# Optimization experiments

Measured on AMD Instinct MI355X. Metric: run time of the kernel, lower is better.

## Reference

```python
import jax, jax.numpy as jnp
import numpy as np

B, L, H, NH = 4, 1024, 768, 12
NE, M, P = 30, 6, 600
EMB, BS, NC = 768, 16, 97
NEG = -1e30


def setup_inputs() -> dict:
    key = jax.random.key(0)
    ks = jax.random.split(key, 9)
    sequence_output = jax.random.normal(ks[0], (B, L, H), jnp.float32)
    attention = jax.random.uniform(ks[1], (B, NH, L, L), jnp.float32)
    mention_idx = jax.random.randint(ks[2], (B, NE, M), 0, L)
    mention_mask = jnp.ones((B, NE, M), jnp.float32)
    hts = jax.random.randint(ks[3], (B, P, 2), 0, NE)
    s = 0.02
    head_W = jax.random.normal(ks[4], (EMB, 2 * H), jnp.float32) * s
    head_b = jnp.zeros((EMB,), jnp.float32)
    tail_W = jax.random.normal(ks[5], (EMB, 2 * H), jnp.float32) * s
    tail_b = jnp.zeros((EMB,), jnp.float32)
    proj_W = jax.random.normal(ks[6], (H, EMB * BS), jnp.float32) * s
    cls_W = jax.random.normal(ks[7], (NC, H), jnp.float32) * s
    cls_b = jnp.zeros((NC,), jnp.float32)
    return {
        'sequence_output': sequence_output, 'attention': attention,
        'head_W': head_W, 'head_b': head_b, 'tail_W': tail_W, 'tail_b': tail_b,
        'proj_W': proj_W, 'cls_W': cls_W, 'cls_b': cls_b,
        'mention_mask': mention_mask, 'mention_idx': mention_idx, 'hts': hts,
    }


def reference(sequence_output, attention, head_W, head_b, tail_W, tail_b,
              proj_W, cls_W, cls_b, mention_mask, mention_idx, hts):
    b_, l_, h_ = sequence_output.shape
    bidx = jnp.arange(b_)[:, None, None]                     # [B,1,1]
    # ---- per-entity pooling (segment reduce over ragged mentions) ----
    m_emb = sequence_output[bidx, mention_idx]               # [B,NE,M,H]
    att_t = attention.transpose(0, 2, 1, 3)                  # [B,L,NH,L]
    m_att = att_t[bidx, mention_idx]                         # [B,NE,M,NH,L]
    masked = jnp.where(mention_mask[..., None] > 0, m_emb, NEG)
    e_emb = jax.nn.logsumexp(masked, axis=2)                 # [B,NE,H]
    cnt = jnp.maximum(mention_mask.sum(2), 1.0)              # [B,NE]
    e_att = (m_att * mention_mask[..., None, None]).sum(2) / cnt[..., None, None]  # [B,NE,NH,L]
    # ---- head/tail gathers over pairs ----
    b2 = jnp.arange(b_)[:, None]                             # [B,1]
    h_emb = e_emb[b2, hts[..., 0]]                           # [B,P,H]
    t_emb = e_emb[b2, hts[..., 1]]
    h_att = e_att[b2, hts[..., 0]]                           # [B,P,NH,L]
    t_att = e_att[b2, hts[..., 1]]
    ht_att = (h_att * t_att).mean(2)                         # [B,P,L]
    ht_att = ht_att / (ht_att.sum(-1, keepdims=True) + 1e-30)
    rs = jnp.einsum('bpl,blh->bph', ht_att, sequence_output) # [B,P,H]
    # ---- extractors + block-bilinear classifier ----
    hs = jnp.tanh(jnp.concatenate([h_emb, rs], -1) @ head_W.T + head_b)  # [B,P,EMB]
    ts = jnp.tanh(jnp.concatenate([t_emb, rs], -1) @ tail_W.T + tail_b)
    emb = hs.shape[-1]
    bs = proj_W.shape[1] // emb
    p_ = hs.shape[1]
    b1 = hs.reshape(b_, p_, emb // bs, bs)
    b2t = ts.reshape(b_, p_, emb // bs, bs)
    bl = (b1[..., :, None] * b2t[..., None, :]).reshape(b_, p_, emb * bs)
    logits = (bl @ proj_W.T) @ cls_W.T + cls_b               # [B,P,NC]
    return logits
```

## Files before the change

kernel.cpp:

```cpp
#include <hip/hip_runtime.h>
#include <cmath>

#define B_   4
#define L_   1024
#define H_   768
#define NH_  12
#define NE_  30
#define M_   6
#define P_   600
#define EMB_ 768
#define BS_  16
#define NC_  97

typedef __bf16 bf16x8 __attribute__((ext_vector_type(8)));
typedef float floatx4 __attribute__((ext_vector_type(4)));

union V16 { uint4 q; __bf16 b[8]; bf16x8 v; };
union V8  { unsigned long long u; __bf16 b[4]; };


__global__ __launch_bounds__(256) void k_entity_pool(
    const float* __restrict__ seq, const float* __restrict__ mmask,
    const int* __restrict__ midx, __bf16* __restrict__ e_embB)
{
  int be = blockIdx.x;
  int tid = threadIdx.x;
  int idx[M_]; float msk[M_];
#pragma unroll
  for (int m = 0; m < M_; ++m) {
    idx[m] = midx[be * M_ + m];
    msk[m] = mmask[be * M_ + m];
  }
  int b = be / NE_;
  const float* sb = seq + (size_t)b * L_ * H_;
  for (int h = tid; h < H_; h += 256) {
    float v[M_]; float mx = -3.0e38f;
#pragma unroll
    for (int m = 0; m < M_; ++m) {
      float x = (msk[m] > 0.f) ? sb[(size_t)idx[m] * H_ + h] : -1e30f;
      v[m] = x; mx = fmaxf(mx, x);
    }
    float s = 0.f;
#pragma unroll
    for (int m = 0; m < M_; ++m) s += expf(v[m] - mx);
    e_embB[(size_t)be * H_ + h] = (__bf16)(mx + logf(s));
  }
}

__global__ __launch_bounds__(256) void k_entity_att(
    const float* __restrict__ att, const float* __restrict__ mmask,
    const int* __restrict__ midx, __bf16* __restrict__ e_att)
{
  int i = blockIdx.x * 256 + threadIdx.x;
  int l4 = (i & 255) * 4;
  int nh = (i >> 8) % NH_;
  int be = i / (256 * NH_);
  int b  = be / NE_;
  float s0=0.f, s1=0.f, s2=0.f, s3=0.f, cnt=0.f;
#pragma unroll
  for (int m = 0; m < M_; ++m) {
    float mk = mmask[be*M_ + m];
    cnt += mk;
    int id = midx[be*M_ + m];
    float4 a = *reinterpret_cast<const float4*>(
        att + (((size_t)b*NH_ + nh)*L_ + id)*L_ + l4);
    s0 += mk*a.x; s1 += mk*a.y; s2 += mk*a.z; s3 += mk*a.w;
  }
  float inv = 1.f / fmaxf(cnt, 1.f);
  V8 o;
  o.b[0]=(__bf16)(s0*inv); o.b[1]=(__bf16)(s1*inv);
  o.b[2]=(__bf16)(s2*inv); o.b[3]=(__bf16)(s3*inv);
  *reinterpret_cast<unsigned long long*>(e_att + ((size_t)be*NH_ + nh)*L_ + l4) = o.u;
}

__global__ __launch_bounds__(256) void k_htatt(
    const __bf16* __restrict__ e_att, const int* __restrict__ hts,
    __bf16* __restrict__ htatt)
{
  int bp = blockIdx.x;
  int b = bp / P_;
  int tid = threadIdx.x;
  int hi = hts[bp*2 + 0], ti = hts[bp*2 + 1];
  const __bf16* ha = e_att + (size_t)(b*NE_ + hi) * NH_ * L_;
  const __bf16* ta = e_att + (size_t)(b*NE_ + ti) * NH_ * L_;
  int l4 = tid * 4;
  float v[4] = {0.f,0.f,0.f,0.f};
#pragma unroll
  for (int nh = 0; nh < NH_; ++nh) {
    V8 x, y;
    x.u = *reinterpret_cast<const unsigned long long*>(ha + nh*L_ + l4);
    y.u = *reinterpret_cast<const unsigned long long*>(ta + nh*L_ + l4);
#pragma unroll
    for (int q = 0; q < 4; ++q) v[q] += (float)x.b[q] * (float)y.b[q];
  }
  float loc = 0.f;
#pragma unroll
  for (int q = 0; q < 4; ++q) { v[q] *= (1.f/NH_); loc += v[q]; }
  __shared__ float red[4];
  for (int off = 32; off > 0; off >>= 1) loc += __shfl_down(loc, off, 64);
  if ((tid & 63) == 0) red[tid >> 6] = loc;
  __syncthreads();
  float inv = 1.f / (red[0] + red[1] + red[2] + red[3] + 1e-30f);
  V8 o;
#pragma unroll
  for (int q = 0; q < 4; ++q) o.b[q] = (__bf16)(v[q] * inv);
  *reinterpret_cast<unsigned long long*>(htatt + (size_t)bp*L_ + l4) = o.u;
}

__global__ __launch_bounds__(256) void k_cvt_weights(
    const float* __restrict__ headW, const float* __restrict__ tailW,
    const float* __restrict__ clsW, __bf16* __restrict__ Wt,
    __bf16* __restrict__ clsA)
{
  int gid = blockIdx.x*256 + threadIdx.x;
  if (gid < 2*H_*384) {
    int sel = gid / (H_*384);
    int rem = gid % (H_*384);
    int o = rem / 384;
    int k4 = (rem % 384) * 4;
    const float* W = sel ? tailW : headW;
    float4 v = *reinterpret_cast<const float4*>(W + (long)o*(2*H_) + k4);
    V8 d; d.b[0]=(__bf16)v.x; d.b[1]=(__bf16)v.y; d.b[2]=(__bf16)v.z; d.b[3]=(__bf16)v.w;
    *reinterpret_cast<unsigned long long*>(Wt + ((long)sel*H_ + o)*(2*H_) + k4) = d.u;
  } else {
    int rem = gid - 2*H_*384;
    int row = rem / 192;
    int k4 = (rem % 192) * 4;
    V8 d;
    if (row < NC_) {
      float4 v = *reinterpret_cast<const float4*>(clsW + (long)row*H_ + k4);
      d.b[0]=(__bf16)v.x; d.b[1]=(__bf16)v.y; d.b[2]=(__bf16)v.z; d.b[3]=(__bf16)v.w;
    } else {
      d.b[0]=d.b[1]=d.b[2]=d.b[3]=(__bf16)0.f;
    }
    *reinterpret_cast<unsigned long long*>(clsA + (long)row*H_ + k4) = d.u;
  }
}

__global__ __launch_bounds__(256) void k_transpose_bf(
    const float* __restrict__ in, __bf16* __restrict__ out,
    int R, int C, long inStride, long outStride)
{
  __shared__ float t[32][33];
  long ib = (long)blockIdx.z * inStride, ob = (long)blockIdx.z * outStride;
  int c0 = blockIdx.x*32, r0 = blockIdx.y*32;
  int tx = threadIdx.x & 31, ty = threadIdx.x >> 5;
#pragma unroll
  for (int p = 0; p < 4; ++p)
    t[ty + p*8][tx] = in[ib + (long)(r0 + ty + p*8)*C + c0 + tx];
  __syncthreads();
#pragma unroll
  for (int p = 0; p < 4; ++p)
    out[ob + (long)(c0 + ty + p*8)*R + r0 + tx] = (__bf16)t[tx][ty + p*8];
}

__device__ __forceinline__ void gemm_core(
    const __bf16* __restrict__ A, int lda, long aRow0,
    const __bf16* __restrict__ Bt, int ldb, long bRow0,
    int K, __bf16* sm, floatx4 acc[2][2])
{
  const int tid = threadIdx.x;
  const int lid = tid & 63, w = tid >> 6;
  const int ar = (w & 1) * 32, bc = (w >> 1) * 32;
  const int frow = lid & 15, kg = lid >> 4;
  __bf16* As = sm;
  __bf16* Bs = sm + 64*40;
  const int srow = tid >> 2, skq = (tid & 3) * 8;
  const __bf16* ag = A + (aRow0 + srow) * (long)lda + skq;
  const __bf16* bg = Bt + (bRow0 + srow) * (long)ldb + skq;
  for (int k0 = 0; k0 < K; k0 += 32) {
    uint4 av = *reinterpret_cast<const uint4*>(ag + k0);
    uint4 bv = *reinterpret_cast<const uint4*>(bg + k0);
    __syncthreads();
    *reinterpret_cast<uint4*>(As + srow*40 + skq) = av;
    *reinterpret_cast<uint4*>(Bs + srow*40 + skq) = bv;
    __syncthreads();
    V16 a0, a1, b0, b1;
    a0.q = *reinterpret_cast<const uint4*>(As + (ar + frow)*40 + kg*8);
    a1.q = *reinterpret_cast<const uint4*>(As + (ar + 16 + frow)*40 + kg*8);
    b0.q = *reinterpret_cast<const uint4*>(Bs + (bc + frow)*40 + kg*8);
    b1.q = *reinterpret_cast<const uint4*>(Bs + (bc + 16 + frow)*40 + kg*8);
    acc[0][0] = __builtin_amdgcn_mfma_f32_16x16x32_bf16(a0.v, b0.v, acc[0][0], 0, 0, 0);
    acc[0][1] = __builtin_amdgcn_mfma_f32_16x16x32_bf16(a0.v, b1.v, acc[0][1], 0, 0, 0);
    acc[1][0] = __builtin_amdgcn_mfma_f32_16x16x32_bf16(a1.v, b0.v, acc[1][0], 0, 0, 0);
    acc[1][1] = __builtin_amdgcn_mfma_f32_16x16x32_bf16(a1.v, b1.v, acc[1][1], 0, 0, 0);
  }
}

__global__ __launch_bounds__(256) void k_rs_mfma(
    const __bf16* __restrict__ htatt, const __bf16* __restrict__ seqT,
    __bf16* __restrict__ rs)
{
  __shared__ __bf16 sm[2*64*40];
  int b = blockIdx.z, p0 = blockIdx.y*64, h0 = blockIdx.x*64;
  floatx4 acc[2][2] = {};
  gemm_core(htatt, L_, (long)b*P_ + p0, seqT + (long)b*H_*L_, L_, h0, L_, sm, acc);
  int lid = threadIdx.x & 63, w = threadIdx.x >> 6;
  int ar = (w&1)*32, bc = (w>>1)*32, frow = lid&15, kg = lid>>4;
#pragma unroll
  for (int i = 0; i < 2; ++i)
#pragma unroll
    for (int r = 0; r < 4; ++r) {
      int p = p0 + ar + i*16 + kg*4 + r;
      if (p < P_) {
#pragma unroll
        for (int j = 0; j < 2; ++j)
          rs[((long)b*P_ + p)*H_ + h0 + bc + j*16 + frow] = (__bf16)acc[i][j][r];
      }
    }
}

__global__ __launch_bounds__(256) void k_pre_mfma(
    const __bf16* __restrict__ e_embB, const __bf16* __restrict__ Wt,
    float* __restrict__ hpre, float* __restrict__ tpre)
{
  __shared__ __bf16 sm[2*64*40];
  int sel = blockIdx.z, r0 = blockIdx.y*64, o0 = blockIdx.x*64;
  floatx4 acc[2][2] = {};
  gemm_core(e_embB, H_, r0, Wt + (long)sel*H_*(2*H_), 2*H_, o0, H_, sm, acc);
  float* out = sel ? tpre : hpre;
  int lid = threadIdx.x & 63, w = threadIdx.x >> 6;
  int ar = (w&1)*32, bc = (w>>1)*32, frow = lid&15, kg = lid>>4;
#pragma unroll
  for (int i = 0; i < 2; ++i)
#pragma unroll
    for (int r = 0; r < 4; ++r) {
      int be = r0 + ar + i*16 + kg*4 + r;
      if (be < B_*NE_) {
#pragma unroll
        for (int j = 0; j < 2; ++j)
          out[(long)be*EMB_ + o0 + bc + j*16 + frow] = acc[i][j][r];
      }
    }
}

__global__ __launch_bounds__(256) void k_extract_mfma(
    const __bf16* __restrict__ rs, const __bf16* __restrict__ Wt,
    const float* __restrict__ headb, const float* __restrict__ tailb,
    const float* __restrict__ hpre, const float* __restrict__ tpre,
    const int* __restrict__ hts, __bf16* __restrict__ hs, __bf16* __restrict__ ts)
{
  __shared__ __bf16 sm[2*64*40];
  int sel = blockIdx.z, r0 = blockIdx.y*64, o0 = blockIdx.x*64;
  const float* bias = sel ? tailb : headb;
  const float* pre = sel ? tpre : hpre;
  __bf16* out = sel ? ts : hs;
  floatx4 acc[2][2] = {};
  gemm_core(rs, H_, r0, Wt + (long)sel*H_*(2*H_) + H_, 2*H_, o0, H_, sm, acc);
  int lid = threadIdx.x & 63, w = threadIdx.x >> 6;
  int ar = (w&1)*32, bc = (w>>1)*32, frow = lid&15, kg = lid>>4;
#pragma unroll
  for (int i = 0; i < 2; ++i)
#pragma unroll
    for (int r = 0; r < 4; ++r) {
      int row = r0 + ar + i*16 + kg*4 + r;
      if (row < B_*P_) {
        int b = row / P_;
        int e = hts[row*2 + sel];
        const float* prow = pre + (long)(b*NE_ + e) * EMB_;
#pragma unroll
        for (int j = 0; j < 2; ++j) {
          int o = o0 + bc + j*16 + frow;
          out[(long)row*EMB_ + o] = (__bf16)tanhf(acc[i][j][r] + prow[o] + bias[o]);
        }
      }
    }
}

__global__ __launch_bounds__(256) void k_wc_mfma(
    const __bf16* __restrict__ clsA, const __bf16* __restrict__ projWT,
    __bf16* __restrict__ WcT)
{
  __shared__ __bf16 sm[2*64*40];
  int n0 = blockIdx.x*64, r0 = blockIdx.y*64;
  floatx4 acc[2][2] = {};
  gemm_core(clsA, H_, r0, projWT, H_, n0, H_, sm, acc);
  int lid = threadIdx.x & 63, w = threadIdx.x >> 6;
  int ar = (w&1)*32, bc = (w>>1)*32, frow = lid&15, kg = lid>>4;
#pragma unroll
  for (int i = 0; i < 2; ++i)
#pragma unroll
    for (int r = 0; r < 4; ++r) {
      int c = r0 + ar + i*16 + kg*4 + r;
#pragma unroll
      for (int j = 0; j < 2; ++j)
        WcT[(long)c*(EMB_*BS_) + n0 + bc + j*16 + frow] = (__bf16)acc[i][j][r];
    }
}

__global__ __launch_bounds__(512) void k_logits_mfma(
    const __bf16* __restrict__ hs, const __bf16* __restrict__ ts,
    const __bf16* __restrict__ WcT, float* __restrict__ partial)
{
  int r0 = blockIdx.x * 16;
  int kh = blockIdx.y;
  int tid = threadIdx.x;
  int w = tid >> 6, lid = tid & 63;
  int frow = lid & 15, kg = lid >> 4;
  int row = r0 + frow;
  long hsrow = (long)row * EMB_;
  floatx4 acc[7] = {};
  int kbase0 = kh*3072 + w*384;
  for (int s = 0; s < 12; ++s) {
    int kb = kbase0 + s*32 + kg*8;
    int q16 = (kb >> 8) << 4;
    int ii = (kb >> 4) & 15;
    int jj0 = kb & 15;
    float hv = (float)hs[hsrow + q16 + ii];
    V16 tsv; tsv.q = *reinterpret_cast<const uint4*>(ts + hsrow + q16 + jj0);
    bf16x8 af;
#pragma unroll
    for (int j = 0; j < 8; ++j) af[j] = (__bf16)(hv * (float)tsv.b[j]);
#pragma unroll
    for (int f = 0; f < 7; ++f) {
      V16 bv; bv.q = *reinterpret_cast<const uint4*>(WcT + (long)(f*16 + frow)*(EMB_*BS_) + kb);
      acc[f] = __builtin_amdgcn_mfma_f32_16x16x32_bf16(af, bv.v, acc[f], 0, 0, 0);
    }
  }
  __shared__ float red[8][16][112];
#pragma unroll
  for (int f = 0; f < 7; ++f)
#pragma unroll
    for (int r = 0; r < 4; ++r)
      red[w][kg*4 + r][f*16 + frow] = acc[f][r];
  __syncthreads();
  for (int e = tid; e < 16*112; e += 512) {
    int rr = e / 112, cc = e % 112;
    float s = 0.f;
#pragma unroll
    for (int ww = 0; ww < 8; ++ww) s += red[ww][rr][cc];
    partial[((long)kh*B_*P_ + r0 + rr)*112 + cc] = s;
  }
}

__global__ __launch_bounds__(256) void k_lred(
    const float* __restrict__ partial, const float* __restrict__ clsb,
    float* __restrict__ out)
{
  int gid = blockIdx.x*256 + threadIdx.x;
  if (gid >= B_*P_*112) return;
  int row = gid / 112, c = gid % 112;
  if (c < NC_) {
    float s = clsb[c];
#pragma unroll
    for (int q = 0; q < 4; ++q)
      s += partial[((long)q*B_*P_ + row)*112 + c];
    out[(long)row*NC_ + c] = s;
  }
}

extern "C" void kernel_launch(void* const* d_in, const int* in_sizes, int n_in,
                              void* d_out, int out_size, void* d_ws, size_t ws_size,
                              hipStream_t stream) {
  const float* seq   = (const float*)d_in[0];
  const float* att   = (const float*)d_in[1];
  const float* headW = (const float*)d_in[2];
  const float* headb = (const float*)d_in[3];
  const float* tailW = (const float*)d_in[4];
  const float* tailb = (const float*)d_in[5];
  const float* projW = (const float*)d_in[6];
  const float* clsW  = (const float*)d_in[7];
  const float* clsb  = (const float*)d_in[8];
  const float* mmask = (const float*)d_in[9];
  const int* midx = (const int*)d_in[10];
  const int* hts  = (const int*)d_in[11];

  char* p = (char*)d_ws;
  auto alloc_f = [&](size_t n){ float* r = (float*)p; p += n*sizeof(float); return r; };
  auto alloc_b = [&](size_t n){ __bf16* r = (__bf16*)p; p += n*2; return r; };
  float* hpre    = alloc_f((size_t)B_*NE_*EMB_);
  float* tpre    = alloc_f((size_t)B_*NE_*EMB_);
  float* partial = alloc_f((size_t)4*B_*P_*112);
  __bf16* e_embB = alloc_b((size_t)128*H_);
  __bf16* e_att  = alloc_b((size_t)B_*NE_*NH_*L_);
  __bf16* htattb = alloc_b((size_t)2464*L_);
  __bf16* seqT   = alloc_b((size_t)B_*H_*L_);
  __bf16* rsb    = alloc_b((size_t)2432*H_);
  __bf16* Wt     = alloc_b((size_t)2*H_*2*H_);
  __bf16* clsA   = alloc_b((size_t)128*H_);
  __bf16* WcT    = alloc_b((size_t)128*EMB_*BS_);
  __bf16* projWT = alloc_b((size_t)EMB_*BS_*H_);
  __bf16* hsb = projWT;
  __bf16* tsb = projWT + (size_t)B_*P_*EMB_;

  k_cvt_weights<<<2400, 256, 0, stream>>>(headW, tailW, clsW, Wt, clsA);
  k_transpose_bf<<<dim3(EMB_*BS_/32, H_/32, 1), 256, 0, stream>>>(
      projW, projWT, H_, EMB_*BS_, 0, 0);
  k_wc_mfma<<<dim3(EMB_*BS_/64, 2), 256, 0, stream>>>(clsA, projWT, WcT);
  k_entity_pool<<<B_*NE_, 256, 0, stream>>>(seq, mmask, midx, e_embB);
  k_entity_att<<<(B_*NE_*NH_*256)/256, 256, 0, stream>>>(att, mmask, midx, e_att);
  k_transpose_bf<<<dim3(H_/32, L_/32, B_), 256, 0, stream>>>(
      seq, seqT, L_, H_, (long)L_*H_, (long)H_*L_);
  k_htatt<<<B_*P_, 256, 0, stream>>>(e_att, hts, htattb);
  k_rs_mfma<<<dim3(H_/64, 10, B_), 256, 0, stream>>>(htattb, seqT, rsb);
  k_pre_mfma<<<dim3(EMB_/64, 2, 2), 256, 0, stream>>>(e_embB, Wt, hpre, tpre);
  k_extract_mfma<<<dim3(EMB_/64, 38, 2), 256, 0, stream>>>(
      rsb, Wt, headb, tailb, hpre, tpre, hts, hsb, tsb);
  k_logits_mfma<<<dim3(150, 4), 512, 0, stream>>>(hsb, tsb, WcT, partial);
  k_lred<<<(B_*P_*112 + 255)/256, 256, 0, stream>>>(partial, clsb, (float*)d_out);
}
```

Measured before the change: 455.2 us.

## Merge independent prep and mid stages into combined kernels; drop logits split-K reduction

```diff
diff --git a/kernel.cpp b/kernel.cpp
--- a/kernel.cpp
+++ b/kernel.cpp
@@ -17,142 +17,6 @@
 
 union V16 { uint4 q; __bf16 b[8]; bf16x8 v; };
 union V8  { unsigned long long u; __bf16 b[4]; };
-
-
-__global__ __launch_bounds__(256) void k_entity_pool(
-    const float* __restrict__ seq, const float* __restrict__ mmask,
-    const int* __restrict__ midx, __bf16* __restrict__ e_embB)
-{
-  int be = blockIdx.x;
-  int tid = threadIdx.x;
-  int idx[M_]; float msk[M_];
-#pragma unroll
-  for (int m = 0; m < M_; ++m) {
-    idx[m] = midx[be * M_ + m];
-    msk[m] = mmask[be * M_ + m];
-  }
-  int b = be / NE_;
-  const float* sb = seq + (size_t)b * L_ * H_;
-  for (int h = tid; h < H_; h += 256) {
-    float v[M_]; float mx = -3.0e38f;
-#pragma unroll
-    for (int m = 0; m < M_; ++m) {
-      float x = (msk[m] > 0.f) ? sb[(size_t)idx[m] * H_ + h] : -1e30f;
-      v[m] = x; mx = fmaxf(mx, x);
-    }
-    float s = 0.f;
-#pragma unroll
-    for (int m = 0; m < M_; ++m) s += expf(v[m] - mx);
-    e_embB[(size_t)be * H_ + h] = (__bf16)(mx + logf(s));
-  }
-}
-
-__global__ __launch_bounds__(256) void k_entity_att(
-    const float* __restrict__ att, const float* __restrict__ mmask,
-    const int* __restrict__ midx, __bf16* __restrict__ e_att)
-{
-  int i = blockIdx.x * 256 + threadIdx.x;
-  int l4 = (i & 255) * 4;
-  int nh = (i >> 8) % NH_;
-  int be = i / (256 * NH_);
-  int b  = be / NE_;
-  float s0=0.f, s1=0.f, s2=0.f, s3=0.f, cnt=0.f;
-#pragma unroll
-  for (int m = 0; m < M_; ++m) {
-    float mk = mmask[be*M_ + m];
-    cnt += mk;
-    int id = midx[be*M_ + m];
-    float4 a = *reinterpret_cast<const float4*>(
-        att + (((size_t)b*NH_ + nh)*L_ + id)*L_ + l4);
-    s0 += mk*a.x; s1 += mk*a.y; s2 += mk*a.z; s3 += mk*a.w;
-  }
-  float inv = 1.f / fmaxf(cnt, 1.f);
-  V8 o;
-  o.b[0]=(__bf16)(s0*inv); o.b[1]=(__bf16)(s1*inv);
-  o.b[2]=(__bf16)(s2*inv); o.b[3]=(__bf16)(s3*inv);
-  *reinterpret_cast<unsigned long long*>(e_att + ((size_t)be*NH_ + nh)*L_ + l4) = o.u;
-}
-
-__global__ __launch_bounds__(256) void k_htatt(
-    const __bf16* __restrict__ e_att, const int* __restrict__ hts,
-    __bf16* __restrict__ htatt)
-{
-  int bp = blockIdx.x;
-  int b = bp / P_;
-  int tid = threadIdx.x;
-  int hi = hts[bp*2 + 0], ti = hts[bp*2 + 1];
-  const __bf16* ha = e_att + (size_t)(b*NE_ + hi) * NH_ * L_;
-  const __bf16* ta = e_att + (size_t)(b*NE_ + ti) * NH_ * L_;
-  int l4 = tid * 4;
-  float v[4] = {0.f,0.f,0.f,0.f};
-#pragma unroll
-  for (int nh = 0; nh < NH_; ++nh) {
-    V8 x, y;
-    x.u = *reinterpret_cast<const unsigned long long*>(ha + nh*L_ + l4);
-    y.u = *reinterpret_cast<const unsigned long long*>(ta + nh*L_ + l4);
-#pragma unroll
-    for (int q = 0; q < 4; ++q) v[q] += (float)x.b[q] * (float)y.b[q];
-  }
-  float loc = 0.f;
-#pragma unroll
-  for (int q = 0; q < 4; ++q) { v[q] *= (1.f/NH_); loc += v[q]; }
-  __shared__ float red[4];
-  for (int off = 32; off > 0; off >>= 1) loc += __shfl_down(loc, off, 64);
-  if ((tid & 63) == 0) red[tid >> 6] = loc;
-  __syncthreads();
-  float inv = 1.f / (red[0] + red[1] + red[2] + red[3] + 1e-30f);
-  V8 o;
-#pragma unroll
-  for (int q = 0; q < 4; ++q) o.b[q] = (__bf16)(v[q] * inv);
-  *reinterpret_cast<unsigned long long*>(htatt + (size_t)bp*L_ + l4) = o.u;
-}
-
-__global__ __launch_bounds__(256) void k_cvt_weights(
-    const float* __restrict__ headW, const float* __restrict__ tailW,
-    const float* __restrict__ clsW, __bf16* __restrict__ Wt,
-    __bf16* __restrict__ clsA)
-{
-  int gid = blockIdx.x*256 + threadIdx.x;
-  if (gid < 2*H_*384) {
-    int sel = gid / (H_*384);
-    int rem = gid % (H_*384);
-    int o = rem / 384;
-    int k4 = (rem % 384) * 4;
-    const float* W = sel ? tailW : headW;
-    float4 v = *reinterpret_cast<const float4*>(W + (long)o*(2*H_) + k4);
-    V8 d; d.b[0]=(__bf16)v.x; d.b[1]=(__bf16)v.y; d.b[2]=(__bf16)v.z; d.b[3]=(__bf16)v.w;
-    *reinterpret_cast<unsigned long long*>(Wt + ((long)sel*H_ + o)*(2*H_) + k4) = d.u;
-  } else {
-    int rem = gid - 2*H_*384;
-    int row = rem / 192;
-    int k4 = (rem % 192) * 4;
-    V8 d;
-    if (row < NC_) {
-      float4 v = *reinterpret_cast<const float4*>(clsW + (long)row*H_ + k4);
-      d.b[0]=(__bf16)v.x; d.b[1]=(__bf16)v.y; d.b[2]=(__bf16)v.z; d.b[3]=(__bf16)v.w;
-    } else {
-      d.b[0]=d.b[1]=d.b[2]=d.b[3]=(__bf16)0.f;
-    }
-    *reinterpret_cast<unsigned long long*>(clsA + (long)row*H_ + k4) = d.u;
-  }
-}
-
-__global__ __launch_bounds__(256) void k_transpose_bf(
-    const float* __restrict__ in, __bf16* __restrict__ out,
-    int R, int C, long inStride, long outStride)
-{
-  __shared__ float t[32][33];
-  long ib = (long)blockIdx.z * inStride, ob = (long)blockIdx.z * outStride;
-  int c0 = blockIdx.x*32, r0 = blockIdx.y*32;
-  int tx = threadIdx.x & 31, ty = threadIdx.x >> 5;
-#pragma unroll
-  for (int p = 0; p < 4; ++p)
-    t[ty + p*8][tx] = in[ib + (long)(r0 + ty + p*8)*C + c0 + tx];
-  __syncthreads();
-#pragma unroll
-  for (int p = 0; p < 4; ++p)
-    out[ob + (long)(c0 + ty + p*8)*R + r0 + tx] = (__bf16)t[tx][ty + p*8];
-}
 
 __device__ __forceinline__ void gemm_core(
     const __bf16* __restrict__ A, int lda, long aRow0,
@@ -187,6 +51,197 @@
   }
 }
 
+#define S1_CVT  2400
+#define S1_TPW  9216
+#define S1_TPS  3072
+#define S1_POOL 120
+#define S1_ATT  1440
+
+__device__ __forceinline__ void transpose_body(
+    const float* __restrict__ in, __bf16* __restrict__ out,
+    int R, int C, int bx, int by, float (*t)[33])
+{
+  int c0 = bx*32, r0 = by*32;
+  int tx = threadIdx.x & 31, ty = threadIdx.x >> 5;
+#pragma unroll
+  for (int p = 0; p < 4; ++p)
+    t[ty + p*8][tx] = in[(long)(r0 + ty + p*8)*C + c0 + tx];
+  __syncthreads();
+#pragma unroll
+  for (int p = 0; p < 4; ++p)
+    out[(long)(c0 + ty + p*8)*R + r0 + tx] = (__bf16)t[tx][ty + p*8];
+}
+
+__global__ __launch_bounds__(256) void k_prep(
+    const float* __restrict__ seq, const float* __restrict__ att,
+    const float* __restrict__ headW, const float* __restrict__ tailW,
+    const float* __restrict__ projW, const float* __restrict__ clsW,
+    const float* __restrict__ mmask, const int* __restrict__ midx,
+    __bf16* __restrict__ Wt, __bf16* __restrict__ clsA,
+    __bf16* __restrict__ projWT, __bf16* __restrict__ seqT,
+    __bf16* __restrict__ e_embB, __bf16* __restrict__ e_att)
+{
+  __shared__ float t[32][33];
+  int blk = blockIdx.x;
+  int tid = threadIdx.x;
+  if (blk < S1_CVT) {
+    int gid = blk*256 + tid;
+    if (gid < 2*H_*384) {
+      int sel = gid / (H_*384);
+      int rem = gid % (H_*384);
+      int o = rem / 384;
+      int k4 = (rem % 384) * 4;
+      const float* W = sel ? tailW : headW;
+      float4 v = *reinterpret_cast<const float4*>(W + (long)o*(2*H_) + k4);
+      V8 d; d.b[0]=(__bf16)v.x; d.b[1]=(__bf16)v.y; d.b[2]=(__bf16)v.z; d.b[3]=(__bf16)v.w;
+      *reinterpret_cast<unsigned long long*>(Wt + ((long)sel*H_ + o)*(2*H_) + k4) = d.u;
+    } else {
+      int rem = gid - 2*H_*384;
+      int row = rem / 192;
+      int k4 = (rem % 192) * 4;
+      V8 d;
+      if (row < NC_) {
+        float4 v = *reinterpret_cast<const float4*>(clsW + (long)row*H_ + k4);
+        d.b[0]=(__bf16)v.x; d.b[1]=(__bf16)v.y; d.b[2]=(__bf16)v.z; d.b[3]=(__bf16)v.w;
+      } else {
+        d.b[0]=d.b[1]=d.b[2]=d.b[3]=(__bf16)0.f;
+      }
+      *reinterpret_cast<unsigned long long*>(clsA + (long)row*H_ + k4) = d.u;
+    }
+  } else if (blk < S1_CVT + S1_TPW) {
+    int b = blk - S1_CVT;
+    transpose_body(projW, projWT, H_, EMB_*BS_, b % 384, b / 384, t);
+  } else if (blk < S1_CVT + S1_TPW + S1_TPS) {
+    int b = blk - (S1_CVT + S1_TPW);
+    int bx = b % 24, by = (b / 24) % 32, bz = b / (24*32);
+    transpose_body(seq + (long)bz*L_*H_, seqT + (long)bz*H_*L_, L_, H_, bx, by, t);
+  } else if (blk < S1_CVT + S1_TPW + S1_TPS + S1_POOL) {
+    int be = blk - (S1_CVT + S1_TPW + S1_TPS);
+    int idx[M_]; float msk[M_];
+#pragma unroll
+    for (int m = 0; m < M_; ++m) {
+      idx[m] = midx[be * M_ + m];
+      msk[m] = mmask[be * M_ + m];
+    }
+    int b = be / NE_;
+    const float* sb = seq + (size_t)b * L_ * H_;
+    for (int h = tid; h < H_; h += 256) {
+      float v[M_]; float mx = -3.0e38f;
+#pragma unroll
+      for (int m = 0; m < M_; ++m) {
+        float x = (msk[m] > 0.f) ? sb[(size_t)idx[m] * H_ + h] : -1e30f;
+        v[m] = x; mx = fmaxf(mx, x);
+      }
+      float s = 0.f;
+#pragma unroll
+      for (int m = 0; m < M_; ++m) s += expf(v[m] - mx);
+      e_embB[(size_t)be * H_ + h] = (__bf16)(mx + logf(s));
+    }
+  } else {
+    int i = (blk - (S1_CVT + S1_TPW + S1_TPS + S1_POOL))*256 + tid;
+    int l4 = (i & 255) * 4;
+    int nh = (i >> 8) % NH_;
+    int be = i / (256 * NH_);
+    int b  = be / NE_;
+    float s0=0.f, s1=0.f, s2=0.f, s3=0.f, cnt=0.f;
+#pragma unroll
+    for (int m = 0; m < M_; ++m) {
+      float mk = mmask[be*M_ + m];
+      cnt += mk;
+      int id = midx[be*M_ + m];
+      float4 a = *reinterpret_cast<const float4*>(
+          att + (((size_t)b*NH_ + nh)*L_ + id)*L_ + l4);
+      s0 += mk*a.x; s1 += mk*a.y; s2 += mk*a.z; s3 += mk*a.w;
+    }
+    float inv = 1.f / fmaxf(cnt, 1.f);
+    V8 o;
+    o.b[0]=(__bf16)(s0*inv); o.b[1]=(__bf16)(s1*inv);
+    o.b[2]=(__bf16)(s2*inv); o.b[3]=(__bf16)(s3*inv);
+    *reinterpret_cast<unsigned long long*>(e_att + ((size_t)be*NH_ + nh)*L_ + l4) = o.u;
+  }
+}
+
+#define S2_WC  384
+#define S2_HT  2400
+#define S2_PRE 48
+
+__global__ __launch_bounds__(256) void k_mid(
+    const __bf16* __restrict__ clsA, const __bf16* __restrict__ projWT,
+    const __bf16* __restrict__ e_att, const int* __restrict__ hts,
+    const __bf16* __restrict__ e_embB, const __bf16* __restrict__ Wt,
+    __bf16* __restrict__ WcT, __bf16* __restrict__ htatt,
+    float* __restrict__ hpre, float* __restrict__ tpre)
+{
+  __shared__ __bf16 sm[2*64*40];
+  int blk = blockIdx.x;
+  int tid = threadIdx.x;
+  if (blk < S2_WC) {
+    int n0 = (blk % 192)*64, r0 = (blk / 192)*64;
+    floatx4 acc[2][2] = {};
+    gemm_core(clsA, H_, r0, projWT, H_, n0, H_, sm, acc);
+    int lid = tid & 63, w = tid >> 6;
+    int ar = (w&1)*32, bc = (w>>1)*32, frow = lid&15, kg = lid>>4;
+#pragma unroll
+    for (int i = 0; i < 2; ++i)
+#pragma unroll
+      for (int r = 0; r < 4; ++r) {
+        int c = r0 + ar + i*16 + kg*4 + r;
+#pragma unroll
+        for (int j = 0; j < 2; ++j)
+          WcT[(long)c*(EMB_*BS_) + n0 + bc + j*16 + frow] = (__bf16)acc[i][j][r];
+      }
+  } else if (blk < S2_WC + S2_HT) {
+    int bp = blk - S2_WC;
+    int b = bp / P_;
+    int hi = hts[bp*2 + 0], ti = hts[bp*2 + 1];
+    const __bf16* ha = e_att + (size_t)(b*NE_ + hi) * NH_ * L_;
+    const __bf16* ta = e_att + (size_t)(b*NE_ + ti) * NH_ * L_;
+    int l4 = tid * 4;
+    float v[4] = {0.f,0.f,0.f,0.f};
+#pragma unroll
+    for (int nh = 0; nh < NH_; ++nh) {
+      V8 x, y;
+      x.u = *reinterpret_cast<const unsigned long long*>(ha + nh*L_ + l4);
+      y.u = *reinterpret_cast<const unsigned long long*>(ta + nh*L_ + l4);
+#pragma unroll
+      for (int q = 0; q < 4; ++q) v[q] += (float)x.b[q] * (float)y.b[q];
+    }
+    float loc = 0.f;
+#pragma unroll
+    for (int q = 0; q < 4; ++q) { v[q] *= (1.f/NH_); loc += v[q]; }
+    float* red = reinterpret_cast<float*>(sm);
+    for (int off = 32; off > 0; off >>= 1) loc += __shfl_down(loc, off, 64);
+    if ((tid & 63) == 0) red[tid >> 6] = loc;
+    __syncthreads();
+    float inv = 1.f / (red[0] + red[1] + red[2] + red[3] + 1e-30f);
+    V8 o;
+#pragma unroll
+    for (int q = 0; q < 4; ++q) o.b[q] = (__bf16)(v[q] * inv);
+    *reinterpret_cast<unsigned long long*>(htatt + (size_t)bp*L_ + l4) = o.u;
+  } else {
+    int tb = blk - (S2_WC + S2_HT);
+    int o0 = (tb % 12)*64;
+    int r0 = ((tb / 12) & 1)*64;
+    int sel = tb / 24;
+    floatx4 acc[2][2] = {};
+    gemm_core(e_embB, H_, r0, Wt + (long)sel*H_*(2*H_), 2*H_, o0, H_, sm, acc);
+    float* out = sel ? tpre : hpre;
+    int lid = tid & 63, w = tid >> 6;
+    int ar = (w&1)*32, bc = (w>>1)*32, frow = lid&15, kg = lid>>4;
+#pragma unroll
+    for (int i = 0; i < 2; ++i)
+#pragma unroll
+      for (int r = 0; r < 4; ++r) {
+        int be = r0 + ar + i*16 + kg*4 + r;
+        if (be < B_*NE_) {
+#pragma unroll
+          for (int j = 0; j < 2; ++j)
+            out[(long)be*EMB_ + o0 + bc + j*16 + frow] = acc[i][j][r];
+        }
+      }
+  }
+}
+
 __global__ __launch_bounds__(256) void k_rs_mfma(
     const __bf16* __restrict__ htatt, const __bf16* __restrict__ seqT,
     __bf16* __restrict__ rs)
@@ -206,30 +261,6 @@
 #pragma unroll
         for (int j = 0; j < 2; ++j)
           rs[((long)b*P_ + p)*H_ + h0 + bc + j*16 + frow] = (__bf16)acc[i][j][r];
-      }
-    }
-}
-
-__global__ __launch_bounds__(256) void k_pre_mfma(
-    const __bf16* __restrict__ e_embB, const __bf16* __restrict__ Wt,
-    float* __restrict__ hpre, float* __restrict__ tpre)
-{
-  __shared__ __bf16 sm[2*64*40];
-  int sel = blockIdx.z, r0 = blockIdx.y*64, o0 = blockIdx.x*64;
-  floatx4 acc[2][2] = {};
-  gemm_core(e_embB, H_, r0, Wt + (long)sel*H_*(2*H_), 2*H_, o0, H_, sm, acc);
-  float* out = sel ? tpre : hpre;
-  int lid = threadIdx.x & 63, w = threadIdx.x >> 6;
-  int ar = (w&1)*32, bc = (w>>1)*32, frow = lid&15, kg = lid>>4;
-#pragma unroll
-  for (int i = 0; i < 2; ++i)
-#pragma unroll
-    for (int r = 0; r < 4; ++r) {
-      int be = r0 + ar + i*16 + kg*4 + r;
-      if (be < B_*NE_) {
-#pragma unroll
-        for (int j = 0; j < 2; ++j)
-          out[(long)be*EMB_ + o0 + bc + j*16 + frow] = acc[i][j][r];
       }
     }
 }
@@ -267,41 +298,20 @@
     }
 }
 
-__global__ __launch_bounds__(256) void k_wc_mfma(
-    const __bf16* __restrict__ clsA, const __bf16* __restrict__ projWT,
-    __bf16* __restrict__ WcT)
-{
-  __shared__ __bf16 sm[2*64*40];
-  int n0 = blockIdx.x*64, r0 = blockIdx.y*64;
-  floatx4 acc[2][2] = {};
-  gemm_core(clsA, H_, r0, projWT, H_, n0, H_, sm, acc);
-  int lid = threadIdx.x & 63, w = threadIdx.x >> 6;
-  int ar = (w&1)*32, bc = (w>>1)*32, frow = lid&15, kg = lid>>4;
-#pragma unroll
-  for (int i = 0; i < 2; ++i)
-#pragma unroll
-    for (int r = 0; r < 4; ++r) {
-      int c = r0 + ar + i*16 + kg*4 + r;
-#pragma unroll
-      for (int j = 0; j < 2; ++j)
-        WcT[(long)c*(EMB_*BS_) + n0 + bc + j*16 + frow] = (__bf16)acc[i][j][r];
-    }
-}
-
 __global__ __launch_bounds__(512) void k_logits_mfma(
     const __bf16* __restrict__ hs, const __bf16* __restrict__ ts,
-    const __bf16* __restrict__ WcT, float* __restrict__ partial)
+    const __bf16* __restrict__ WcT, const float* __restrict__ clsb,
+    float* __restrict__ out)
 {
   int r0 = blockIdx.x * 16;
-  int kh = blockIdx.y;
   int tid = threadIdx.x;
   int w = tid >> 6, lid = tid & 63;
   int frow = lid & 15, kg = lid >> 4;
   int row = r0 + frow;
   long hsrow = (long)row * EMB_;
   floatx4 acc[7] = {};
-  int kbase0 = kh*3072 + w*384;
-  for (int s = 0; s < 12; ++s) {
+  int kbase0 = w*1536;
+  for (int s = 0; s < 48; ++s) {
     int kb = kbase0 + s*32 + kg*8;
     int q16 = (kb >> 8) << 4;
     int ii = (kb >> 4) & 15;
@@ -326,26 +336,12 @@
   __syncthreads();
   for (int e = tid; e < 16*112; e += 512) {
     int rr = e / 112, cc = e % 112;
-    float s = 0.f;
-#pragma unroll
-    for (int ww = 0; ww < 8; ++ww) s += red[ww][rr][cc];
-    partial[((long)kh*B_*P_ + r0 + rr)*112 + cc] = s;
-  }
-}
-
-__global__ __launch_bounds__(256) void k_lred(
-    const float* __restrict__ partial, const float* __restrict__ clsb,
-    float* __restrict__ out)
-{
-  int gid = blockIdx.x*256 + threadIdx.x;
-  if (gid >= B_*P_*112) return;
-  int row = gid / 112, c = gid % 112;
-  if (c < NC_) {
-    float s = clsb[c];
-#pragma unroll
-    for (int q = 0; q < 4; ++q)
-      s += partial[((long)q*B_*P_ + row)*112 + c];
-    out[(long)row*NC_ + c] = s;
+    if (cc < NC_) {
+      float s = clsb[cc];
+#pragma unroll
+      for (int ww = 0; ww < 8; ++ww) s += red[ww][rr][cc];
+      out[(long)(r0 + rr)*NC_ + cc] = s;
+    }
   }
 }
 
@@ -370,7 +366,6 @@
   auto alloc_b = [&](size_t n){ __bf16* r = (__bf16*)p; p += n*2; return r; };
   float* hpre    = alloc_f((size_t)B_*NE_*EMB_);
   float* tpre    = alloc_f((size_t)B_*NE_*EMB_);
-  float* partial = alloc_f((size_t)4*B_*P_*112);
   __bf16* e_embB = alloc_b((size_t)128*H_);
   __bf16* e_att  = alloc_b((size_t)B_*NE_*NH_*L_);
   __bf16* htattb = alloc_b((size_t)2464*L_);
@@ -383,19 +378,13 @@
   __bf16* hsb = projWT;
   __bf16* tsb = projWT + (size_t)B_*P_*EMB_;
 
-  k_cvt_weights<<<2400, 256, 0, stream>>>(headW, tailW, clsW, Wt, clsA);
-  k_transpose_bf<<<dim3(EMB_*BS_/32, H_/32, 1), 256, 0, stream>>>(
-      projW, projWT, H_, EMB_*BS_, 0, 0);
-  k_wc_mfma<<<dim3(EMB_*BS_/64, 2), 256, 0, stream>>>(clsA, projWT, WcT);
-  k_entity_pool<<<B_*NE_, 256, 0, stream>>>(seq, mmask, midx, e_embB);
-  k_entity_att<<<(B_*NE_*NH_*256)/256, 256, 0, stream>>>(att, mmask, midx, e_att);
-  k_transpose_bf<<<dim3(H_/32, L_/32, B_), 256, 0, stream>>>(
-      seq, seqT, L_, H_, (long)L_*H_, (long)H_*L_);
-  k_htatt<<<B_*P_, 256, 0, stream>>>(e_att, hts, htattb);
+  k_prep<<<S1_CVT + S1_TPW + S1_TPS + S1_POOL + S1_ATT, 256, 0, stream>>>(
+      seq, att, headW, tailW, projW, clsW, mmask, midx,
+      Wt, clsA, projWT, seqT, e_embB, e_att);
+  k_mid<<<S2_WC + S2_HT + S2_PRE, 256, 0, stream>>>(
+      clsA, projWT, e_att, hts, e_embB, Wt, WcT, htattb, hpre, tpre);
   k_rs_mfma<<<dim3(H_/64, 10, B_), 256, 0, stream>>>(htattb, seqT, rsb);
-  k_pre_mfma<<<dim3(EMB_/64, 2, 2), 256, 0, stream>>>(e_embB, Wt, hpre, tpre);
   k_extract_mfma<<<dim3(EMB_/64, 38, 2), 256, 0, stream>>>(
       rsb, Wt, headb, tailb, hpre, tpre, hts, hsb, tsb);
-  k_logits_mfma<<<dim3(150, 4), 512, 0, stream>>>(hsb, tsb, WcT, partial);
-  k_lred<<<(B_*P_*112 + 255)/256, 256, 0, stream>>>(partial, clsb, (float*)d_out);
-}
+  k_logits_mfma<<<150, 512, 0, stream>>>(hsb, tsb, WcT, clsb, (float*)d_out);
+}
```

Measured after the change: 451.7 us. Within noise of the previous version (-0.8%).
